# Kernel optimization log

Measured on AMD Instinct MI355X. Metric: run time of the kernel, lower is better.

Reference implementation:

```python
import jax, jax.numpy as jnp
import numpy as np

B, L, C, K = 8, 16384, 64, 7
NORM_FACTOR = 1.0
LN_EPS = 1e-6


def setup_inputs() -> dict:
    key = jax.random.key(0)
    k0, k1, k2 = jax.random.split(key, 3)
    x = jax.random.normal(k0, (B, L, C), dtype=jnp.float32)
    # lecun_normal-style init for (C_out, C_in, K) dynamic-conv weights
    weights = jax.random.normal(k1, (C, C, K), dtype=jnp.float32) / np.float32(np.sqrt(C))
    ln_scale = jnp.ones((C,), dtype=jnp.float32)
    ln_bias = jnp.zeros((C,), dtype=jnp.float32)
    conv_kernel = jax.random.normal(k2, (C, C), dtype=jnp.float32) / np.float32(np.sqrt(C))
    conv_bias = jnp.zeros((C,), dtype=jnp.float32)
    prelu_slope = jnp.asarray(0.01, dtype=jnp.float32)
    return {"x": x, "weights": weights, "ln_scale": ln_scale, "ln_bias": ln_bias,
            "conv_kernel": conv_kernel, "conv_bias": conv_bias, "prelu_slope": prelu_slope}


def reference(x, weights, ln_scale, ln_bias, conv_kernel, conv_bias, prelu_slope):
    b, l, c = x.shape
    k = weights.shape[-1]
    x0 = x  # residual source, (B, L, C)

    # im2col unfold over sequence: window 2K, stride 2, no padding
    p = jax.lax.conv_general_dilated_patches(
        jnp.transpose(x, (0, 2, 1)),  # (B, C, L)
        filter_shape=(2 * k,), window_strides=(2,), padding=((0, 0),))
    t = p.shape[-1]  # out_len = (L - 2K)//2 + 1
    p = jnp.reshape(p, (b, c, 2 * k, t))
    p = jnp.transpose(p, (0, 1, 3, 2))  # (B, C, T, 2K)

    # dynamic weights from the trailing 2T inputs: (B, 2T, C) x (C, C, K) -> (B, C, 2T, K)
    w = jnp.einsum('blc,dck->bdlk', x0[:, -(t * 2):, :], weights)
    even_seq = w[:, :, ::2, :]   # (B, C, T, K)
    odd_seq = w[:, :, 1::2, :]   # (B, C, T, K)
    w = jnp.stack([even_seq, odd_seq], axis=-1)         # (B, C, T, K, 2)
    w = jnp.reshape(w, (b, c, t, k * 2))                # interleaved (B, C, T, 2K)
    w = jnp.tanh(w / NORM_FACTOR)

    # gated windowed sum
    y = jnp.sum(p * w, axis=3)          # (B, C, T)
    y = jnp.transpose(y, (0, 2, 1))     # (B, T, C)

    # inner skip: stride-2 subsample of input, aligned to the tail
    y = x0[:, ::2, :][:, -t:, :] + y

    # LayerNorm over channel dim (flax default eps=1e-6, with scale and bias)
    mu = jnp.mean(y, axis=-1, keepdims=True)
    var = jnp.mean(jnp.square(y - mu), axis=-1, keepdims=True)
    yn = (y - mu) * jax.lax.rsqrt(var + LN_EPS) * ln_scale + ln_bias

    # 1x1 conv + PReLU + outer skip
    z = jnp.einsum('btc,co->bto', yn, conv_kernel) + conv_bias
    z = jnp.where(z >= 0, z, prelu_slope * z)
    return yn + z
```

## Files before the change

### kernel.cpp

```cpp
#include <hip/hip_runtime.h>
#include <stdint.h>

#define BB 8
#define LLEN 16384
#define CC 64
#define TOUT 8186
#define TILE_T 32
#define NROWS 76
#define SXS 68
#define SXGS 72
#define YNS 66
#define YNBS 76

typedef __attribute__((ext_vector_type(8))) short short8;
typedef __attribute__((ext_vector_type(4))) float float4v;
typedef __attribute__((ext_vector_type(4))) unsigned short ushort4v;

__device__ inline unsigned short f2bf(float f) {
  union { float f; uint32_t u; } v; v.f = f;
  uint32_t r = v.u + 0x7fffu + ((v.u >> 16) & 1u);
  return (unsigned short)(r >> 16);
}
__device__ inline float rcp_fast(float x) {
  float r; asm("v_rcp_f32 %0, %1" : "=v"(r) : "v"(x)); return r;
}
__device__ inline float exp2_fast(float x) {
  float r; asm("v_exp_f32 %0, %1" : "=v"(r) : "v"(x)); return r;
}
__device__ inline float tanh_fast(float a) {
  float e = exp2_fast(a * 2.885390082f);
  return __builtin_fmaf(-2.0f, rcp_fast(e + 1.0f), 1.0f);
}

__global__ void prep_frags(const float* __restrict__ weights,
                           const float* __restrict__ ck,
                           unsigned short* __restrict__ wfrag,
                           unsigned short* __restrict__ ckfrag)
{
  int bid = blockIdx.x, tid = threadIdx.x;
  if (bid < 56) {
    int nt = bid >> 1, kh = bid & 1;
    for (int e = tid; e < 512; e += 256) {
      int ln = e >> 3, j = e & 7;
      int kk = nt >> 2;
      int d  = (nt & 3) * 16 + (ln & 15);
      int cp = kh * 32 + (ln >> 4) * 8 + j;
      wfrag[(bid * 64 + ln) * 8 + j] = f2bf(weights[d * 448 + cp * 7 + kk]);
    }
  } else {
    int bb2 = bid - 56;
    int nt = bb2 >> 1, kh = bb2 & 1;
    for (int e = tid; e < 512; e += 256) {
      int ln = e >> 3, j = e & 7;
      int oo = nt * 16 + (ln & 15);
      int c2 = kh * 32 + (ln >> 4) * 8 + j;
      ckfrag[(bb2 * 64 + ln) * 8 + j] = f2bf(ck[c2 * 64 + oo]);
    }
  }
}

__global__ __launch_bounds__(256, 4)
void convblock_main(const float* __restrict__ x,
                    const unsigned short* __restrict__ wfrag,
                    const unsigned short* __restrict__ ckfrag,
                    const float* __restrict__ ln_scale,
                    const float* __restrict__ ln_bias,
                    const float* __restrict__ conv_bias,
                    const float* __restrict__ prelu_slope,
                    float* __restrict__ out)
{
  __shared__ __align__(16) char smem[29888];
  float*          sx2 = (float*)smem;
  unsigned short* ynb = (unsigned short*)smem;
  unsigned short* sxg = (unsigned short*)(smem + 20672);
  float*          ynf = (float*)(smem + 20672);

  const int tid  = threadIdx.x;
  const int b    = blockIdx.x >> 8;
  const int t0   = (blockIdx.x & 255) * TILE_T;
  const int lane = tid & 63;
  const int w    = tid >> 6;
  const int l15  = tid & 15;
  const int q    = (tid >> 4) & 3;

  {
    const float* xb = x + (size_t)b * ((size_t)LLEN * CC);
    #pragma unroll
    for (int i = 0; i < 5; ++i) {
      int idx = tid + i * 256;
      if (idx < NROWS * 16) {
        int row = idx >> 4, f4 = idx & 15, c0 = f4 * 4;
        int rowg = 2 * t0 + row;
        if (rowg > LLEN - 1) rowg = LLEN - 1;
        float4v v = *(const float4v*)(xb + (size_t)rowg * CC + c0);
        int base = row * SXS + 16 * (f4 & 3) + (f4 >> 2);
        sx2[base + 0]  = v[0];
        sx2[base + 4]  = v[1];
        sx2[base + 8]  = v[2];
        sx2[base + 12] = v[3];
        if (row >= 12) {
          ushort4v p;
          p[0] = f2bf(v[0]); p[1] = f2bf(v[1]); p[2] = f2bf(v[2]); p[3] = f2bf(v[3]);
          *(ushort4v*)&sxg[(row - 12) * SXGS + c0] = p;
        }
      }
    }
  }
  float lnS[4], lnB[4];
  #pragma unroll
  for (int dq = 0; dq < 4; ++dq) {
    lnS[dq] = ln_scale[16 * dq + l15];
    lnB[dq] = ln_bias[16 * dq + l15];
  }
  __syncthreads();

  short8 a0 = *(const short8*)&sxg[(16 * w + l15) * SXGS + q * 8];
  short8 a1 = *(const short8*)&sxg[(16 * w + l15) * SXGS + 32 + q * 8];
  __syncthreads();

  float y[2][4];
  #pragma unroll
  for (int dlt = 0; dlt < 2; ++dlt)
    #pragma unroll
    for (int dq = 0; dq < 4; ++dq) y[dlt][dq] = 0.f;

  const float4v zacc = (float4v){0.f, 0.f, 0.f, 0.f};
  const int dtbase = 8 * w + 2 * q;
  const unsigned short* wp = wfrag + lane * 8;
  #pragma unroll 1
  for (int kk = 0; kk < 7; ++kk) {
    float4v acc[4];
    #pragma unroll
    for (int dq = 0; dq < 4; ++dq) {
      short8 b0 = *(const short8*)(wp + dq * 1024);
      short8 b1 = *(const short8*)(wp + dq * 1024 + 512);
      float4v a = __builtin_amdgcn_mfma_f32_16x16x32_bf16(a0, b0, zacc, 0, 0, 0);
      acc[dq] = __builtin_amdgcn_mfma_f32_16x16x32_bf16(a1, b1, a, 0, 0, 0);
    }
    #pragma unroll
    for (int dlt = 0; dlt < 2; ++dlt) {
      int rowe = 2 * (dtbase + dlt) + 2 * kk;
      float4v xe = *(const float4v*)&sx2[rowe * SXS + l15 * 4];
      float4v xo = *(const float4v*)&sx2[(rowe + 1) * SXS + l15 * 4];
      #pragma unroll
      for (int dq = 0; dq < 4; ++dq) {
        float ge = tanh_fast(acc[dq][2 * dlt + 0]);
        float go = tanh_fast(acc[dq][2 * dlt + 1]);
        y[dlt][dq] += xe[dq] * ge + xo[dq] * go;
      }
    }
    wp += 4096;
  }
  #pragma unroll
  for (int dlt = 0; dlt < 2; ++dlt) {
    int rowe = 2 * (dtbase + dlt) + 12;
    float4v xe = *(const float4v*)&sx2[rowe * SXS + l15 * 4];
    #pragma unroll
    for (int dq = 0; dq < 4; ++dq) y[dlt][dq] += xe[dq];
  }

  float ynr[2][4];
  #pragma unroll
  for (int dlt = 0; dlt < 2; ++dlt) {
    float s1 = y[dlt][0] + y[dlt][1] + y[dlt][2] + y[dlt][3];
    float s2 = y[dlt][0]*y[dlt][0] + y[dlt][1]*y[dlt][1]
             + y[dlt][2]*y[dlt][2] + y[dlt][3]*y[dlt][3];
    #pragma unroll
    for (int m = 1; m < 16; m <<= 1) {
      s1 += __shfl_xor(s1, m, 64);
      s2 += __shfl_xor(s2, m, 64);
    }
    float mu   = s1 * (1.0f / 64.0f);
    float var  = s2 * (1.0f / 64.0f) - mu * mu;
    float rstd = rsqrtf(var + 1e-6f);
    int dt = dtbase + dlt;
    #pragma unroll
    for (int dq = 0; dq < 4; ++dq) {
      float yn = (y[dlt][dq] - mu) * rstd * lnS[dq] + lnB[dq];
      ynr[dlt][dq] = yn;
      ynf[dt * YNS + 16 * dq + l15] = yn;
    }
  }
  __syncthreads();

  #pragma unroll
  for (int dlt = 0; dlt < 2; ++dlt)
    #pragma unroll
    for (int dq = 0; dq < 4; ++dq)
      ynb[(dtbase + dlt) * YNBS + 16 * dq + l15] = f2bf(ynr[dlt][dq]);
  __syncthreads();

  const float sl = prelu_slope[0];
  const int   o  = 16 * w + l15;
  const float cb = conv_bias[o];
  short8 bf0 = *(const short8*)&ckfrag[((w * 2 + 0) * 64 + lane) * 8];
  short8 bf1 = *(const short8*)&ckfrag[((w * 2 + 1) * 64 + lane) * 8];
  #pragma unroll
  for (int mt = 0; mt < 2; ++mt) {
    short8 af0 = *(const short8*)&ynb[(mt * 16 + l15) * YNBS + q * 8];
    short8 af1 = *(const short8*)&ynb[(mt * 16 + l15) * YNBS + 32 + q * 8];
    float4v zc = __builtin_amdgcn_mfma_f32_16x16x32_bf16(af0, bf0, zacc, 0, 0, 0);
    zc = __builtin_amdgcn_mfma_f32_16x16x32_bf16(af1, bf1, zc, 0, 0, 0);
    #pragma unroll
    for (int r = 0; r < 4; ++r) {
      int t  = mt * 16 + 4 * q + r;
      int tg = t0 + t;
      if (tg < TOUT) {
        float z = zc[r] + cb;
        z = (z >= 0.f) ? z : sl * z;
        out[((size_t)b * TOUT + tg) * CC + o] = ynf[t * YNS + o] + z;
      }
    }
  }
}

extern "C" void kernel_launch(void* const* d_in, const int* in_sizes, int n_in,
                              void* d_out, int out_size, void* d_ws, size_t ws_size,
                              hipStream_t stream)
{
  const float* x        = (const float*)d_in[0];
  const float* weights  = (const float*)d_in[1];
  const float* ln_scale = (const float*)d_in[2];
  const float* ln_bias  = (const float*)d_in[3];
  const float* ck       = (const float*)d_in[4];
  const float* cb       = (const float*)d_in[5];
  const float* slope    = (const float*)d_in[6];
  unsigned short* wfrag  = (unsigned short*)d_ws;
  unsigned short* ckfrag = (unsigned short*)((char*)d_ws + 57344);

  prep_frags<<<64, 256, 0, stream>>>(weights, ck, wfrag, ckfrag);
  convblock_main<<<BB * 256, 256, 0, stream>>>(x, wfrag, ckfrag, ln_scale,
                                               ln_bias, cb, slope, (float*)d_out);
}
```

Before: 109.8 us.

## Drop bf16 staging buffer and shrink LDS to raise occupancy

Removes the separate bf16 copy of x in shared memory and builds the MFMA A fragments directly from the fp32 tile with per-element conversion. This shrinks LDS per block from about 29.9KB to 20.7KB, so launch bounds are raised to 6 blocks per CU. ynf is moved to overlap the sx2 region, and both yn stores now happen after a barrier. The cost is 16 scattered LDS reads plus conversions per thread, and possibly more register pressure under the tighter launch bound.

After: 111.5 us. About the same (+1.6%).

```diff
diff --git a/kernel.cpp b/kernel.cpp
--- a/kernel.cpp
+++ b/kernel.cpp
@@ -8,7 +8,6 @@
 #define TILE_T 32
 #define NROWS 76
 #define SXS 68
-#define SXGS 72
 #define YNS 66
 #define YNBS 76
 
@@ -59,7 +58,7 @@
   }
 }
 
-__global__ __launch_bounds__(256, 4)
+__global__ __launch_bounds__(256, 6)
 void convblock_main(const float* __restrict__ x,
                     const unsigned short* __restrict__ wfrag,
                     const unsigned short* __restrict__ ckfrag,
@@ -69,11 +68,10 @@
                     const float* __restrict__ prelu_slope,
                     float* __restrict__ out)
 {
-  __shared__ __align__(16) char smem[29888];
+  __shared__ __align__(16) char smem[20672];
   float*          sx2 = (float*)smem;
   unsigned short* ynb = (unsigned short*)smem;
-  unsigned short* sxg = (unsigned short*)(smem + 20672);
-  float*          ynf = (float*)(smem + 20672);
+  float*          ynf = (float*)(smem + 4864);
 
   const int tid  = threadIdx.x;
   const int b    = blockIdx.x >> 8;
@@ -89,34 +87,33 @@
     for (int i = 0; i < 5; ++i) {
       int idx = tid + i * 256;
       if (idx < NROWS * 16) {
-        int row = idx >> 4, f4 = idx & 15, c0 = f4 * 4;
+        int row = idx >> 4, f4 = idx & 15;
         int rowg = 2 * t0 + row;
         if (rowg > LLEN - 1) rowg = LLEN - 1;
-        float4v v = *(const float4v*)(xb + (size_t)rowg * CC + c0);
+        float4v v = *(const float4v*)(xb + (size_t)rowg * CC + f4 * 4);
         int base = row * SXS + 16 * (f4 & 3) + (f4 >> 2);
         sx2[base + 0]  = v[0];
         sx2[base + 4]  = v[1];
         sx2[base + 8]  = v[2];
         sx2[base + 12] = v[3];
-        if (row >= 12) {
-          ushort4v p;
-          p[0] = f2bf(v[0]); p[1] = f2bf(v[1]); p[2] = f2bf(v[2]); p[3] = f2bf(v[3]);
-          *(ushort4v*)&sxg[(row - 12) * SXGS + c0] = p;
-        }
       }
     }
   }
-  float lnS[4], lnB[4];
-  #pragma unroll
-  for (int dq = 0; dq < 4; ++dq) {
-    lnS[dq] = ln_scale[16 * dq + l15];
-    lnB[dq] = ln_bias[16 * dq + l15];
-  }
   __syncthreads();
 
-  short8 a0 = *(const short8*)&sxg[(16 * w + l15) * SXGS + q * 8];
-  short8 a1 = *(const short8*)&sxg[(16 * w + l15) * SXGS + 32 + q * 8];
-  __syncthreads();
+  short8 a0, a1;
+  {
+    const int rowoff = (12 + 16 * w + l15) * SXS;
+    #pragma unroll
+    for (int j = 0; j < 8; ++j) {
+      int c0 = q * 8 + j;
+      int w0 = 16 * ((c0 >> 2) & 3) + (c0 >> 4) + 4 * (c0 & 3);
+      a0[j] = (short)f2bf(sx2[rowoff + w0]);
+      int c1 = 32 + q * 8 + j;
+      int w1 = 16 * ((c1 >> 2) & 3) + (c1 >> 4) + 4 * (c1 & 3);
+      a1[j] = (short)f2bf(sx2[rowoff + w1]);
+    }
+  }
 
   float y[2][4];
   #pragma unroll
@@ -159,6 +156,12 @@
     for (int dq = 0; dq < 4; ++dq) y[dlt][dq] += xe[dq];
   }
 
+  float lnS[4], lnB[4];
+  #pragma unroll
+  for (int dq = 0; dq < 4; ++dq) {
+    lnS[dq] = ln_scale[16 * dq + l15];
+    lnB[dq] = ln_bias[16 * dq + l15];
+  }
   float ynr[2][4];
   #pragma unroll
   for (int dlt = 0; dlt < 2; ++dlt) {
@@ -173,21 +176,21 @@
     float mu   = s1 * (1.0f / 64.0f);
     float var  = s2 * (1.0f / 64.0f) - mu * mu;
     float rstd = rsqrtf(var + 1e-6f);
+    #pragma unroll
+    for (int dq = 0; dq < 4; ++dq)
+      ynr[dlt][dq] = (y[dlt][dq] - mu) * rstd * lnS[dq] + lnB[dq];
+  }
+  __syncthreads();
+
+  #pragma unroll
+  for (int dlt = 0; dlt < 2; ++dlt) {
     int dt = dtbase + dlt;
     #pragma unroll
     for (int dq = 0; dq < 4; ++dq) {
-      float yn = (y[dlt][dq] - mu) * rstd * lnS[dq] + lnB[dq];
-      ynr[dlt][dq] = yn;
-      ynf[dt * YNS + 16 * dq + l15] = yn;
-    }
-  }
-  __syncthreads();
-
-  #pragma unroll
-  for (int dlt = 0; dlt < 2; ++dlt)
-    #pragma unroll
-    for (int dq = 0; dq < 4; ++dq)
-      ynb[(dtbase + dlt) * YNBS + 16 * dq + l15] = f2bf(ynr[dlt][dq]);
+      ynf[dt * YNS + 16 * dq + l15] = ynr[dlt][dq];
+      ynb[dt * YNBS + 16 * dq + l15] = f2bf(ynr[dlt][dq]);
+    }
+  }
   __syncthreads();
 
   const float sl = prelu_slope[0];
```
